# Performance work log

Hardware: AMD Instinct MI355X
Metric: run time of the kernel (lower is better)

The kernel has to match this reference:

```python
import jax, jax.numpy as jnp
import numpy as np

EPS = 1e-3          # keras BatchNormalization default epsilon
DT = 0.2
LAM2 = 4.0          # lambda_diffusion**2 = 2.0**2
K = 5

def _bn(x, gamma, beta, mean, var):
    # inference-mode batch norm over channel (last) axis
    return (x - mean) * jax.lax.rsqrt(var + EPS) * gamma + beta

def _conv(x, w):
    # NHWC 'same' conv, stride 1, no bias
    return jax.lax.conv_general_dilated(x, w, (1, 1), 'SAME',
                                        dimension_numbers=('NHWC', 'HWIO', 'NHWC'))

def _sobel_edges(x):
    # tf.image.sobel_edges: per-channel 3x3 Sobel with REFLECT padding.
    # returns (dy, dx) matching sobel[...,0], sobel[...,1]
    p = jnp.pad(x, ((0, 0), (1, 1), (1, 1), (0, 0)), mode='reflect')
    dy = (p[:, 2:, :-2] + 2 * p[:, 2:, 1:-1] + p[:, 2:, 2:]) \
       - (p[:, :-2, :-2] + 2 * p[:, :-2, 1:-1] + p[:, :-2, 2:])
    dx = (p[:, :-2, 2:] + 2 * p[:, 1:-1, 2:] + p[:, 2:, 2:]) \
       - (p[:, :-2, :-2] + 2 * p[:, 1:-1, :-2] + p[:, 2:, :-2])
    return dy, dx

def setup_inputs() -> dict:
    key = jax.random.key(0)
    k1, k2, k3 = jax.random.split(key, 3)
    B, H, W, Cin, Cout = 16, 128, 128, 64, 64
    c = jnp.float32
    return {
        'x':   jax.random.normal(k1, (B, H, W, Cin), dtype=c),
        'f_w': jax.random.normal(k2, (3, 3, Cin, Cout), dtype=c) * 0.05,
        'g_w': jax.random.normal(k3, (3, 3, Cout, Cout), dtype=c) * 0.05,
        'bnf_gamma': jnp.ones((Cin,), c),  'bnf_beta': jnp.zeros((Cin,), c),
        'bnf_mean':  jnp.zeros((Cin,), c), 'bnf_var':  jnp.ones((Cin,), c),
        'bng_gamma': jnp.ones((Cout,), c), 'bng_beta': jnp.zeros((Cout,), c),
        'bng_mean':  jnp.zeros((Cout,), c),'bng_var':  jnp.ones((Cout,), c),
        'bno_gamma': jnp.ones((Cout,), c), 'bno_beta': jnp.zeros((Cout,), c),
        'bno_mean':  jnp.zeros((Cout,), c),'bno_var':  jnp.ones((Cout,), c),
    }

def reference(x, f_w, g_w,
              bnf_gamma, bnf_beta, bnf_mean, bnf_var,
              bng_gamma, bng_beta, bng_mean, bng_var,
              bno_gamma, bno_beta, bno_mean, bno_var):
    f = _conv(jax.nn.relu(_bn(x, bnf_gamma, bnf_beta, bnf_mean, bnf_var)), f_w)
    h = f
    g = _conv(jax.nn.relu(_bn(h, bng_gamma, bng_beta, bng_mean, bng_var)), g_w)
    g1 = g
    dy, dx = _sobel_edges(h)
    Dx = 1.0 / (dy * dy / LAM2 + 1.0)   # source: sobel[..., 0]
    Dy = 1.0 / (dx * dx / LAM2 + 1.0)   # source: sobel[..., 1]
    # NOTE: faithful to source — rolls on axis=2 (W) and axis=3 (channels in NHWC)
    ux = 0.5 * (jnp.roll(g, 1, axis=2) - jnp.roll(g, -1, axis=2))
    vy = 0.5 * (jnp.roll(g1, 1, axis=3) - jnp.roll(g1, -1, axis=3))
    Ax = g * DT
    Ay = g1 * DT
    Bx = Dx * DT
    By = Dy * DT
    E = (ux + vy) * DT
    D = 1.0 / (1.0 + 2 * Bx + 2 * By)
    h0 = h
    for _ in range(K):
        prev = h
        h = D * ((1 - 2 * Bx - 2 * By) * h0
                 - 2 * E * h
                 + (-Ax + 2 * Bx) * jnp.roll(h, 1, axis=2)
                 + ( Ax + 2 * Bx) * jnp.roll(h, -1, axis=2)
                 + (-Ay + 2 * By) * jnp.roll(h, 1, axis=3)
                 + ( Ay + 2 * By) * jnp.roll(h, -1, axis=3)
                 + 2 * DT * f)
        h0 = prev
    h = jax.nn.relu(_bn(h, bno_gamma, bno_beta, bno_mean, bno_var))
    return (h, g)
```

## Files before the change

### kernel.cpp

```cpp
#include <hip/hip_runtime.h>

#define HH 128
#define WW 128
#define CC 64
#define ROW (WW*CC)
#define PADW 72

typedef _Float16 half8 __attribute__((ext_vector_type(8)));
typedef _Float16 half4v __attribute__((ext_vector_type(4)));
typedef float floatx4 __attribute__((ext_vector_type(4)));

__device__ inline floatx4 rcp4(floatx4 v)
{
    floatx4 r;
    r[0] = __builtin_amdgcn_rcpf(v[0]);
    r[1] = __builtin_amdgcn_rcpf(v[1]);
    r[2] = __builtin_amdgcn_rcpf(v[2]);
    r[3] = __builtin_amdgcn_rcpf(v[3]);
    return r;
}

__global__ __launch_bounds__(256)
void repack_w(const float* __restrict__ wf, const float* __restrict__ wg,
              _Float16* __restrict__ W2f, _Float16* __restrict__ W2g)
{
    int idx = blockIdx.x * 256 + threadIdx.x;
    int sel = idx >= 36864;
    int id  = sel ? idx - 36864 : idx;
    const float* src = sel ? wg : wf;
    _Float16* dst = sel ? W2g : W2f;
    int t = id >> 12, c = (id >> 6) & 63, o = id & 63;
    int kc = c >> 5, q = (c >> 3) & 3, j = c & 7;
    int pos = ((((t*2 + kc)*4 + q)*64 + o) << 3) + j;
    dst[pos] = (_Float16)src[id];
}

template<int BNIN, int EPI>
__global__ __launch_bounds__(256, 2)
void conv_mfma(const void* __restrict__ srcv, const _Float16* __restrict__ W2,
               _Float16* __restrict__ outH, float* __restrict__ outF,
               _Float16* __restrict__ y2,
               const float* __restrict__ ig, const float* __restrict__ ib,
               const float* __restrict__ imu, const float* __restrict__ iva,
               const float* __restrict__ og, const float* __restrict__ ob,
               const float* __restrict__ om, const float* __restrict__ ov)
{
    __shared__ __align__(16) _Float16 sIn[4*130*PADW];
    const int t = threadIdx.x;
    const int blk = ((blockIdx.x & 7) << 7) | (blockIdx.x >> 3);
    const int b = blk >> 6, i0 = (blk & 63) * 2;

    const int c8 = (t & 7) << 3;
    float scv[8], biv[8];
    if (BNIN) {
        #pragma unroll
        for (int j = 0; j < 8; ++j) {
            float s = ig[c8+j] * rsqrtf(iva[c8+j] + 1e-3f);
            scv[j] = s; biv[j] = ib[c8+j] - imu[c8+j]*s;
        }
    }

    for (int r = 0; r < 4; ++r) {
        int iy = i0 - 1 + r;
        bool inb = (iy >= 0) && (iy < HH);
        #pragma unroll
        for (int k = 0; k < 4; ++k) {
            int idx = t + (k << 8);
            int px = idx >> 3;
            half8 v = {0,0,0,0,0,0,0,0};
            if (inb) {
                if (BNIN) {
                    const float* gp = (const float*)srcv
                        + ((size_t)(b*HH + iy))*ROW + px*CC + c8;
                    float4 u0 = *(const float4*)gp;
                    float4 u1 = *(const float4*)(gp + 4);
                    v[0] = (_Float16)fmaxf(0.f, u0.x*scv[0] + biv[0]);
                    v[1] = (_Float16)fmaxf(0.f, u0.y*scv[1] + biv[1]);
                    v[2] = (_Float16)fmaxf(0.f, u0.z*scv[2] + biv[2]);
                    v[3] = (_Float16)fmaxf(0.f, u0.w*scv[3] + biv[3]);
                    v[4] = (_Float16)fmaxf(0.f, u1.x*scv[4] + biv[4]);
                    v[5] = (_Float16)fmaxf(0.f, u1.y*scv[5] + biv[5]);
                    v[6] = (_Float16)fmaxf(0.f, u1.z*scv[6] + biv[6]);
                    v[7] = (_Float16)fmaxf(0.f, u1.w*scv[7] + biv[7]);
                } else {
                    v = *(const half8*)((const _Float16*)srcv
                        + ((size_t)(b*HH + iy))*ROW + px*CC + c8);
                }
            }
            *(half8*)(sIn + (r*130 + px + 1)*PADW + c8) = v;
        }
    }
    if (t < 128) {
        int rr = t >> 5, s = (t >> 4) & 1, c4 = (t & 15) << 2;
        int slot = s ? 129 : 0;
        half4v z = {0,0,0,0};
        *(half4v*)(sIn + (rr*130 + slot)*PADW + c4) = z;
    }
    __syncthreads();

    const int wv = t >> 6, lane = t & 63;
    const int lm = lane & 15, quad = lane >> 4;
    const int r  = wv >> 1;
    const int px0 = (wv & 1) * 64;
    floatx4 z4 = {0.f,0.f,0.f,0.f};
    floatx4 acc[4][4];
    #pragma unroll
    for (int ms = 0; ms < 4; ++ms)
        #pragma unroll
        for (int nt = 0; nt < 4; ++nt) acc[ms][nt] = z4;

    #pragma unroll
    for (int tap = 0; tap < 9; ++tap) {
        const int di = tap / 3, dj = tap % 3;
        #pragma unroll
        for (int kc = 0; kc < 2; ++kc) {
            const _Float16* ab = sIn + ((r + di)*130 + px0 + lm + dj)*PADW
                               + kc*32 + quad*8;
            half8 a0 = *(const half8*)(ab);
            half8 a1 = *(const half8*)(ab + 16*PADW);
            half8 a2 = *(const half8*)(ab + 32*PADW);
            half8 a3 = *(const half8*)(ab + 48*PADW);
            const _Float16* wb = W2 + (((tap*2 + kc)*4 + quad) << 9) + (lm << 3);
            half8 b0 = *(const half8*)(wb);
            half8 b1 = *(const half8*)(wb + 128);
            half8 b2 = *(const half8*)(wb + 256);
            half8 b3 = *(const half8*)(wb + 384);
            acc[0][0] = __builtin_amdgcn_mfma_f32_16x16x32_f16(a0, b0, acc[0][0], 0,0,0);
            acc[1][0] = __builtin_amdgcn_mfma_f32_16x16x32_f16(a1, b0, acc[1][0], 0,0,0);
            acc[2][0] = __builtin_amdgcn_mfma_f32_16x16x32_f16(a2, b0, acc[2][0], 0,0,0);
            acc[3][0] = __builtin_amdgcn_mfma_f32_16x16x32_f16(a3, b0, acc[3][0], 0,0,0);
            acc[0][1] = __builtin_amdgcn_mfma_f32_16x16x32_f16(a0, b1, acc[0][1], 0,0,0);
            acc[1][1] = __builtin_amdgcn_mfma_f32_16x16x32_f16(a1, b1, acc[1][1], 0,0,0);
            acc[2][1] = __builtin_amdgcn_mfma_f32_16x16x32_f16(a2, b1, acc[2][1], 0,0,0);
            acc[3][1] = __builtin_amdgcn_mfma_f32_16x16x32_f16(a3, b1, acc[3][1], 0,0,0);
            acc[0][2] = __builtin_amdgcn_mfma_f32_16x16x32_f16(a0, b2, acc[0][2], 0,0,0);
            acc[1][2] = __builtin_amdgcn_mfma_f32_16x16x32_f16(a1, b2, acc[1][2], 0,0,0);
            acc[2][2] = __builtin_amdgcn_mfma_f32_16x16x32_f16(a2, b2, acc[2][2], 0,0,0);
            acc[3][2] = __builtin_amdgcn_mfma_f32_16x16x32_f16(a3, b2, acc[3][2], 0,0,0);
            acc[0][3] = __builtin_amdgcn_mfma_f32_16x16x32_f16(a0, b3, acc[0][3], 0,0,0);
            acc[1][3] = __builtin_amdgcn_mfma_f32_16x16x32_f16(a1, b3, acc[1][3], 0,0,0);
            acc[2][3] = __builtin_amdgcn_mfma_f32_16x16x32_f16(a2, b3, acc[2][3], 0,0,0);
            acc[3][3] = __builtin_amdgcn_mfma_f32_16x16x32_f16(a3, b3, acc[3][3], 0,0,0);
        }
    }

    __syncthreads();
    float* sF = (float*)sIn;
    #pragma unroll
    for (int nt = 0; nt < 4; ++nt) {
        int c = nt*16 + lm;
        #pragma unroll
        for (int ms = 0; ms < 4; ++ms) {
            int pix = r*128 + px0 + ms*16 + quad*4;
            floatx4 v = acc[ms][nt];
            #pragma unroll
            for (int rv = 0; rv < 4; ++rv)
                sF[(pix + rv)*64 + c] = v[rv];
        }
    }
    __syncthreads();

    const size_t gbase = ((size_t)(b*HH + i0)) * ROW;
    if (EPI) {
        const int c8o = (t & 7) << 3;
        float s8[8], bb8[8];
        #pragma unroll
        for (int j = 0; j < 8; ++j) {
            float ss = og[c8o+j] * rsqrtf(ov[c8o+j] + 1e-3f);
            s8[j] = ss; bb8[j] = ob[c8o+j] - om[c8o+j]*ss;
        }
        #pragma unroll
        for (int jj = 0; jj < 8; ++jj) {
            int e = (jj*256 + t) << 3;
            floatx4 u0 = *(const floatx4*)(sF + e);
            floatx4 u1 = *(const floatx4*)(sF + e + 4);
            half8 hv, yv;
            #pragma unroll
            for (int j = 0; j < 4; ++j) {
                hv[j]   = (_Float16)u0[j];
                hv[4+j] = (_Float16)u1[j];
                yv[j]   = (_Float16)fmaxf(0.f, u0[j]*s8[j]   + bb8[j]);
                yv[4+j] = (_Float16)fmaxf(0.f, u1[j]*s8[4+j] + bb8[4+j]);
            }
            *(half8*)(outH + gbase + e) = hv;
            *(half8*)(y2   + gbase + e) = yv;
        }
    } else {
        #pragma unroll
        for (int jj = 0; jj < 16; ++jj) {
            int e = (jj*256 + t) << 2;
            *(floatx4*)(outF + gbase + e) = *(const floatx4*)(sF + e);
        }
    }
}

__global__ __launch_bounds__(1024, 2)
void diffuse(const _Float16* __restrict__ f, const float* __restrict__ g,
             float* __restrict__ out,
             const float* __restrict__ bog, const float* __restrict__ bob,
             const float* __restrict__ bom, const float* __restrict__ bov)
{
    __shared__ float B0[ROW], B1[ROW];
    const int t = threadIdx.x;
    const int rowb = ((blockIdx.x & 7) << 8) | (blockIdx.x >> 3);
    const int b = rowb >> 7, i = rowb & 127;
    const int im = (i == 0)    ? 1    : i - 1;
    const int ip = (i == HH-1) ? HH-2 : i + 1;
    const _Float16* fb  = f + (size_t)b * (HH*ROW);
    const _Float16* frm = fb + (size_t)im * ROW;
    const _Float16* fr0 = fb + (size_t)i  * ROW;
    const _Float16* frp = fb + (size_t)ip * ROW;
    const float* grow = g + (size_t)rowb * ROW;

    const int lane = t & 63;
    const int srcm = (lane & 48) | ((lane - 1) & 15);
    const int srcp = (lane & 48) | ((lane + 1) & 15);
    const int w0 = t >> 4, c0 = (t & 15) << 2;
    const int qch[2] = { t*4, t*4 + 4096 };
    const int wch[2] = { w0, w0 + 64 };

    #pragma unroll
    for (int k = 0; k < 2; ++k) {
        half4v vm = *(const half4v*)(frm + qch[k]);
        half4v vp = *(const half4v*)(frp + qch[k]);
        floatx4 a = { (float)vm[0], (float)vm[1], (float)vm[2], (float)vm[3] };
        floatx4 p = { (float)vp[0], (float)vp[1], (float)vp[2], (float)vp[3] };
        *(floatx4*)(B0 + qch[k]) = a;
        *(floatx4*)(B1 + qch[k]) = p;
    }
    __syncthreads();

    floatx4 Bx4[2], dxp4[2];
    #pragma unroll
    for (int k = 0; k < 2; ++k) {
        int w = wch[k];
        int wm = (w == 0)    ? 1      : w - 1;
        int wp = (w == WW-1) ? WW - 2 : w + 1;
        floatx4 am = *(const floatx4*)(B0 + wm*CC + c0);
        floatx4 a0 = *(const floatx4*)(B0 + w *CC + c0);
        floatx4 ap = *(const floatx4*)(B0 + wp*CC + c0);
        floatx4 bm = *(const floatx4*)(B1 + wm*CC + c0);
        floatx4 b0 = *(const floatx4*)(B1 + w *CC + c0);
        floatx4 bp = *(const floatx4*)(B1 + wp*CC + c0);
        floatx4 dy = (bm + 2.f*b0 + bp) - (am + 2.f*a0 + ap);
        Bx4[k]  = 0.2f * rcp4(dy*dy*0.25f + 1.f);
        dxp4[k] = (ap - am) + (bp - bm);
    }
    __syncthreads();

    #pragma unroll
    for (int k = 0; k < 2; ++k) {
        half4v v0 = *(const half4v*)(fr0 + qch[k]);
        floatx4 fv = { (float)v0[0], (float)v0[1], (float)v0[2], (float)v0[3] };
        *(floatx4*)(B0 + qch[k]) = fv;
        *(floatx4*)(B1 + qch[k]) = *(const floatx4*)(grow + qch[k]);
    }
    __syncthreads();

    floatx4 cR4[2], cL4[2], cU4[2], cH0[2], cEE[2], cF[2], h4[2], h04[2];
    #pragma unroll
    for (int k = 0; k < 2; ++k) {
        int w = wch[k];
        int wm = (w == 0)    ? 1      : w - 1;
        int wp = (w == WW-1) ? WW - 2 : w + 1;
        int wl = (w + WW - 1) & (WW - 1);
        int wr = (w + 1) & (WW - 1);
        floatx4 fm = *(const floatx4*)(B0 + wm*CC + c0);
        floatx4 fv = *(const floatx4*)(B0 + w *CC + c0);
        floatx4 fp = *(const floatx4*)(B0 + wp*CC + c0);
        floatx4 dx = dxp4[k] + 2.f*(fp - fm);
        floatx4 By = 0.2f * rcp4(dx*dx*0.25f + 1.f);
        floatx4 Bx = Bx4[k];
        floatx4 gv = *(const floatx4*)(B1 + w *CC + c0);
        floatx4 gl = *(const floatx4*)(B1 + wl*CC + c0);
        floatx4 gr = *(const floatx4*)(B1 + wr*CC + c0);
        float gdm = __shfl(gv[3], srcm, 64);
        float gup = __shfl(gv[0], srcp, 64);
        floatx4 gd = { gdm, gv[0], gv[1], gv[2] };
        floatx4 gu = { gv[1], gv[2], gv[3], gup };
        floatx4 E  = ((gl - gr) + (gd - gu)) * 0.1f;
        floatx4 Dd = rcp4(1.f + 2.f*Bx + 2.f*By);
        floatx4 P  = 2.f * Bx * Dd;
        floatx4 R  = 2.f * By * Dd;
        floatx4 Q  = (gv * 0.2f) * Dd;
        cR4[k] = P + Q;
        cL4[k] = P - Q;
        cU4[k] = R + Q;
        cH0[k] = 2.f*Dd - 1.f;
        cEE[k] = -2.f * E * Dd;
        cF[k]  = 0.4f * Dd * fv;
        h4[k] = fv; h04[k] = fv;
    }
    __syncthreads();

    int oWl[2], oWr[2];
    #pragma unroll
    for (int k = 0; k < 2; ++k) {
        int w = wch[k];
        oWl[k] = ((w + WW - 1) & (WW - 1))*CC + c0;
        oWr[k] = ((w + 1) & (WW - 1))*CC + c0;
    }

    float* cur = B0;
    float* oth = B1;
    for (int it = 0; it < 5; ++it) {
        #pragma unroll
        for (int k = 0; k < 2; ++k) {
            floatx4 hl = *(const floatx4*)(cur + oWl[k]);
            floatx4 hr = *(const floatx4*)(cur + oWr[k]);
            floatx4 hv = h4[k];
            float hdm = __shfl(hv[3], srcm, 64);
            float hup = __shfl(hv[0], srcp, 64);
            floatx4 hd = { hdm, hv[0], hv[1], hv[2] };
            floatx4 hu = { hv[1], hv[2], hv[3], hup };
            floatx4 cD = (cU4[k] - cR4[k]) + cL4[k];
            floatx4 hn = cH0[k]*h04[k] + cEE[k]*hv
                       + cR4[k]*hr + cL4[k]*hl
                       + cU4[k]*hu + cD*hd + cF[k];
            if (it < 4)
                *(floatx4*)(oth + qch[k]) = hn;
            h04[k] = hv; h4[k] = hn;
        }
        if (it < 4) {
            __syncthreads();
            float* tmp = cur; cur = oth; oth = tmp;
        }
    }

    floatx4 gg = *(const floatx4*)(bog + c0);
    floatx4 vv = *(const floatx4*)(bov + c0);
    floatx4 bb = *(const floatx4*)(bob + c0);
    floatx4 mm = *(const floatx4*)(bom + c0);
    floatx4 s4, bi4;
    #pragma unroll
    for (int j = 0; j < 4; ++j) s4[j] = gg[j] * rsqrtf(vv[j] + 1e-3f);
    bi4 = bb - mm*s4;
    float* op = out + (size_t)rowb * ROW;
    #pragma unroll
    for (int k = 0; k < 2; ++k) {
        floatx4 rr = h4[k]*s4 + bi4;
        #pragma unroll
        for (int j = 0; j < 4; ++j) rr[j] = fmaxf(0.f, rr[j]);
        *(floatx4*)(op + qch[k]) = rr;
    }
}

extern "C" void kernel_launch(void* const* d_in, const int* in_sizes, int n_in,
                              void* d_out, int out_size, void* d_ws, size_t ws_size,
                              hipStream_t stream)
{
    const float* x    = (const float*)d_in[0];
    const float* f_w  = (const float*)d_in[1];
    const float* g_w  = (const float*)d_in[2];
    const float* bnf_g = (const float*)d_in[3];
    const float* bnf_b = (const float*)d_in[4];
    const float* bnf_m = (const float*)d_in[5];
    const float* bnf_v = (const float*)d_in[6];
    const float* bng_g = (const float*)d_in[7];
    const float* bng_b = (const float*)d_in[8];
    const float* bng_m = (const float*)d_in[9];
    const float* bng_v = (const float*)d_in[10];
    const float* bno_g = (const float*)d_in[11];
    const float* bno_b = (const float*)d_in[12];
    const float* bno_m = (const float*)d_in[13];
    const float* bno_v = (const float*)d_in[14];

    float* out = (float*)d_out;
    const size_t N = (size_t)16 * HH * WW * CC;
    _Float16* y2   = (_Float16*)d_ws;
    _Float16* fbuf = y2 + N;
    _Float16* W2f  = y2 + 2*N;
    _Float16* W2g  = W2f + 36864;

    repack_w<<<288, 256, 0, stream>>>(f_w, g_w, W2f, W2g);
    conv_mfma<1,1><<<1024, 256, 0, stream>>>(x, W2f, fbuf, nullptr, y2,
                                             bnf_g, bnf_b, bnf_m, bnf_v,
                                             bng_g, bng_b, bng_m, bng_v);
    conv_mfma<0,0><<<1024, 256, 0, stream>>>(y2, W2g, nullptr, out + N, nullptr,
                                             nullptr, nullptr, nullptr, nullptr,
                                             nullptr, nullptr, nullptr, nullptr);
    diffuse<<<2048, 1024, 0, stream>>>(fbuf, out + N, out, bno_g, bno_b, bno_m, bno_v);
}
```

Measured before the change: 323.7 us.

## Swizzle conv LDS layout and stream second-conv input with global_load_lds

Replaces the padded LDS row layout with 128-byte slots that use an XOR swizzle to avoid bank conflicts on the MFMA A-operand reads. The first conv's epilogue writes y2 already pre-swizzled, so the second conv can copy rows straight into LDS with global_load_lds, bypassing registers. The fp32 staging buffer gets a padded stride to reduce conflicts on the epilogue writes and reads. Shared memory grows to 68 KB, which may limit occupancy. Correctness depends on the y2 swizzle matching the read-side key exactly.

```diff
diff --git a/kernel.cpp b/kernel.cpp
--- a/kernel.cpp
+++ b/kernel.cpp
@@ -4,7 +4,9 @@
 #define WW 128
 #define CC 64
 #define ROW (WW*CC)
-#define PADW 72
+#define SLOTB 128
+#define ROWB (130*SLOTB)
+#define FSTR 68
 
 typedef _Float16 half8 __attribute__((ext_vector_type(8)));
 typedef _Float16 half4v __attribute__((ext_vector_type(4)));
@@ -45,7 +47,7 @@
                const float* __restrict__ og, const float* __restrict__ ob,
                const float* __restrict__ om, const float* __restrict__ ov)
 {
-    __shared__ __align__(16) _Float16 sIn[4*130*PADW];
+    __shared__ __align__(16) char smem[69632];
     const int t = threadIdx.x;
     const int blk = ((blockIdx.x & 7) << 7) | (blockIdx.x >> 3);
     const int b = blk >> 6, i0 = (blk & 63) * 2;
@@ -60,16 +62,21 @@
         }
     }
 
-    for (int r = 0; r < 4; ++r) {
-        int iy = i0 - 1 + r;
-        bool inb = (iy >= 0) && (iy < HH);
-        #pragma unroll
-        for (int k = 0; k < 4; ++k) {
-            int idx = t + (k << 8);
-            int px = idx >> 3;
-            half8 v = {0,0,0,0,0,0,0,0};
-            if (inb) {
-                if (BNIN) {
+    {
+        int rr = t >> 6, s = (t >> 5) & 1;
+        *(float*)(smem + rr*ROWB + (s ? 129*SLOTB : 0) + ((t & 31) << 2)) = 0.f;
+    }
+
+    if (BNIN) {
+        for (int r = 0; r < 4; ++r) {
+            int iy = i0 - 1 + r;
+            bool inb = (iy >= 0) && (iy < HH);
+            #pragma unroll
+            for (int k = 0; k < 4; ++k) {
+                int idx = t + (k << 8);
+                int px = idx >> 3;
+                half8 v = {0,0,0,0,0,0,0,0};
+                if (inb) {
                     const float* gp = (const float*)srcv
                         + ((size_t)(b*HH + iy))*ROW + px*CC + c8;
                     float4 u0 = *(const float4*)gp;
@@ -82,19 +89,35 @@
                     v[5] = (_Float16)fmaxf(0.f, u1.y*scv[5] + biv[5]);
                     v[6] = (_Float16)fmaxf(0.f, u1.z*scv[6] + biv[6]);
                     v[7] = (_Float16)fmaxf(0.f, u1.w*scv[7] + biv[7]);
-                } else {
-                    v = *(const half8*)((const _Float16*)srcv
-                        + ((size_t)(b*HH + iy))*ROW + px*CC + c8);
                 }
+                int key = ((px + 1) & 7) << 4;
+                *(half8*)(smem + r*ROWB + (px + 1)*SLOTB
+                          + ((((t & 7) << 4)) ^ key)) = v;
             }
-            *(half8*)(sIn + (r*130 + px + 1)*PADW + c8) = v;
-        }
-    }
-    if (t < 128) {
-        int rr = t >> 5, s = (t >> 4) & 1, c4 = (t & 15) << 2;
-        int slot = s ? 129 : 0;
-        half4v z = {0,0,0,0};
-        *(half4v*)(sIn + (rr*130 + slot)*PADW + c4) = z;
+        }
+    } else {
+        const _Float16* src = (const _Float16*)srcv;
+        #pragma unroll
+        for (int r = 0; r < 4; ++r) {
+            int iy = i0 - 1 + r;
+            char* lb = smem + r*ROWB + SLOTB;
+            if (iy >= 0 && iy < HH) {
+                const _Float16* gp = src + (size_t)(b*HH + iy)*ROW;
+                #pragma unroll
+                for (int k = 0; k < 4; ++k) {
+                    int eo = ((k << 8) + t) << 3;
+                    __builtin_amdgcn_global_load_lds(
+                        (const __attribute__((address_space(1))) void*)(gp + eo),
+                        (__attribute__((address_space(3))) void*)(lb + (eo << 1)),
+                        16, 0, 0);
+                }
+            } else {
+                half8 z = {0,0,0,0,0,0,0,0};
+                #pragma unroll
+                for (int k = 0; k < 4; ++k)
+                    *(half8*)(lb + (((k << 8) + t) << 4)) = z;
+            }
+        }
     }
     __syncthreads();
 
@@ -112,14 +135,16 @@
     #pragma unroll
     for (int tap = 0; tap < 9; ++tap) {
         const int di = tap / 3, dj = tap % 3;
+        const int slot = px0 + lm + dj;
+        const int key  = (slot & 7) << 4;
+        const char* abase = smem + (r + di)*ROWB + slot*SLOTB;
         #pragma unroll
         for (int kc = 0; kc < 2; ++kc) {
-            const _Float16* ab = sIn + ((r + di)*130 + px0 + lm + dj)*PADW
-                               + kc*32 + quad*8;
+            const char* ab = abase + ((kc*64 + quad*16) ^ key);
             half8 a0 = *(const half8*)(ab);
-            half8 a1 = *(const half8*)(ab + 16*PADW);
-            half8 a2 = *(const half8*)(ab + 32*PADW);
-            half8 a3 = *(const half8*)(ab + 48*PADW);
+            half8 a1 = *(const half8*)(ab + 16*SLOTB);
+            half8 a2 = *(const half8*)(ab + 32*SLOTB);
+            half8 a3 = *(const half8*)(ab + 48*SLOTB);
             const _Float16* wb = W2 + (((tap*2 + kc)*4 + quad) << 9) + (lm << 3);
             half8 b0 = *(const half8*)(wb);
             half8 b1 = *(const half8*)(wb + 128);
@@ -145,7 +170,7 @@
     }
 
     __syncthreads();
-    float* sF = (float*)sIn;
+    float* sF = (float*)smem;
     #pragma unroll
     for (int nt = 0; nt < 4; ++nt) {
         int c = nt*16 + lm;
@@ -155,7 +180,7 @@
             floatx4 v = acc[ms][nt];
             #pragma unroll
             for (int rv = 0; rv < 4; ++rv)
-                sF[(pix + rv)*64 + c] = v[rv];
+                sF[(pix + rv)*FSTR + c] = v[rv];
         }
     }
     __syncthreads();
@@ -171,9 +196,11 @@
         }
         #pragma unroll
         for (int jj = 0; jj < 8; ++jj) {
-            int e = (jj*256 + t) << 3;
-            floatx4 u0 = *(const floatx4*)(sF + e);
-            floatx4 u1 = *(const floatx4*)(sF + e + 4);
+            int chunk = jj*256 + t;
+            int px = chunk >> 3;
+            const float* sp = sF + px*FSTR + c8o;
+            floatx4 u0 = *(const floatx4*)(sp);
+            floatx4 u1 = *(const floatx4*)(sp + 4);
             half8 hv, yv;
             #pragma unroll
             for (int j = 0; j < 4; ++j) {
@@ -182,14 +209,21 @@
                 yv[j]   = (_Float16)fmaxf(0.f, u0[j]*s8[j]   + bb8[j]);
                 yv[4+j] = (_Float16)fmaxf(0.f, u1[j]*s8[4+j] + bb8[4+j]);
             }
-            *(half8*)(outH + gbase + e) = hv;
-            *(half8*)(y2   + gbase + e) = yv;
+            size_t oe = gbase + (size_t)px*64 + c8o;
+            *(half8*)(outH + oe) = hv;
+            int key8 = ((px + 1) & 7) << 3;
+            *(half8*)(y2 + gbase + (size_t)px*64 + (c8o ^ key8)) = yv;
         }
     } else {
         #pragma unroll
-        for (int jj = 0; jj < 16; ++jj) {
-            int e = (jj*256 + t) << 2;
-            *(floatx4*)(outF + gbase + e) = *(const floatx4*)(sF + e);
+        for (int jj = 0; jj < 8; ++jj) {
+            int chunk = jj*256 + t;
+            int px = chunk >> 3;
+            const int cc = (t & 7) << 3;
+            const float* sp = sF + px*FSTR + cc;
+            size_t oe = gbase + (size_t)px*64 + cc;
+            *(floatx4*)(outF + oe)     = *(const floatx4*)(sp);
+            *(floatx4*)(outF + oe + 4) = *(const floatx4*)(sp + 4);
         }
     }
 }
```

Result: no change. 321.1 us (-0.8%).
